# Kernel tuning notes

Hardware: AMD Instinct MI355X
Metric: run time of the kernel (lower is better)

Reference implementation:

```python
import jax, jax.numpy as jnp
import numpy as np

N_NODES = 50000
N_EDGES = 800000
D_IN = 256
D_HID = 256
N_LAYERS = 3
N_GRAPHS = 64
LN_EPS = 1e-5


def setup_inputs() -> dict:
    key = jax.random.key(0)
    ks = jax.random.split(key, 8)
    x = jax.random.normal(ks[0], (N_NODES, D_IN), dtype=jnp.float32)
    edge_index = jax.random.randint(ks[1], (2, N_EDGES), 0, N_NODES, dtype=jnp.int32)
    batch = jnp.sort(jax.random.randint(ks[2], (N_NODES,), 0, N_GRAPHS, dtype=jnp.int32))
    # GCNConv weights (glorot-ish) and biases; all layers are [D, D] since in_dim == hidden_dim
    scale = 1.0 / np.sqrt(D_IN)
    Ws = jax.random.normal(ks[3], (N_LAYERS, D_IN, D_HID), dtype=jnp.float32) * scale
    bs = jnp.zeros((N_LAYERS, D_HID), dtype=jnp.float32)
    gammas = jnp.ones((N_LAYERS, D_HID), dtype=jnp.float32)
    betas = jnp.zeros((N_LAYERS, D_HID), dtype=jnp.float32)
    return {"x": x, "edge_index": edge_index, "batch": batch,
            "Ws": Ws, "bs": bs, "gammas": gammas, "betas": betas}


def _gcn_conv(x, W, b, src, dst):
    # PyG GCNConv: h = xW; add self-loops; symmetric deg^{-1/2} normalization; scatter-add; + bias
    h = x @ W  # [N, D]
    deg = jnp.zeros((N_NODES,), dtype=x.dtype).at[dst].add(1.0) + 1.0  # +1 for self-loop
    dinv = jax.lax.rsqrt(deg)  # deg >= 1, safe
    coef = (dinv[src] * dinv[dst])[:, None]  # [E, 1]
    agg = jax.ops.segment_sum(h[src] * coef, dst, num_segments=N_NODES)
    agg = agg + h * (dinv * dinv)[:, None]  # self-loop contribution
    return agg + b


def _layer_norm(x, gamma, beta):
    mu = jnp.mean(x, axis=-1, keepdims=True)
    var = jnp.mean(jnp.square(x - mu), axis=-1, keepdims=True)
    return (x - mu) * jax.lax.rsqrt(var + LN_EPS) * gamma + beta


def reference(x, edge_index, batch, Ws, bs, gammas, betas):
    src, dst = edge_index[0], edge_index[1]
    h = x
    for l in range(N_LAYERS):
        h = _gcn_conv(h, Ws[l], bs[l], src, dst)
        h = _layer_norm(h, gammas[l], betas[l])
        h = jax.nn.relu(h)  # dropout is identity in eval mode
    # global mean pool over graphs
    sums = jax.ops.segment_sum(h, batch, num_segments=N_GRAPHS)  # [B, D]
    counts = jax.ops.segment_sum(jnp.ones((N_NODES,), dtype=h.dtype), batch, num_segments=N_GRAPHS)
    return sums / jnp.maximum(counts, 1.0)[:, None]
```

## Files before the change

### kernel.cpp

```cpp
#include <hip/hip_runtime.h>
#include <hip/hip_bf16.h>

#define N_NODES   50000
#define N_EDGES   800000
#define D         256
#define N_LAYERS  3
#define N_GRAPHS  64
#define LN_EPS    1e-5f
#define NB_SCAN   ((N_NODES + 255) / 256)

typedef __attribute__((ext_vector_type(8))) short bf16x8;
typedef __attribute__((ext_vector_type(4))) float f32x4;

__device__ __forceinline__ unsigned short f2bf(float f) {
    unsigned int u = __float_as_uint(f);
    unsigned int r = (u + 0x7FFFu + ((u >> 16) & 1u)) >> 16;
    return (unsigned short)r;
}
__device__ __forceinline__ float bf2f(unsigned short h) {
    return __uint_as_float(((unsigned int)h) << 16);
}

__global__ void k_xtobf_s(const float* __restrict__ x, const float* __restrict__ dinv,
                          unsigned short* __restrict__ xb) {
    int gid = blockIdx.x * blockDim.x + threadIdx.x;
    int base = gid * 8;
    if (base >= N_NODES * D) return;
    float sc = dinv[base >> 8];
    const float4* x4 = (const float4*)(x + base);
    float4 a = x4[0], b = x4[1];
    ushort4 lo, hi;
    lo.x = f2bf(a.x * sc); lo.y = f2bf(a.y * sc); lo.z = f2bf(a.z * sc); lo.w = f2bf(a.w * sc);
    hi.x = f2bf(b.x * sc); hi.y = f2bf(b.y * sc); hi.z = f2bf(b.z * sc); hi.w = f2bf(b.w * sc);
    ((ushort4*)(xb + base))[0] = lo;
    ((ushort4*)(xb + base))[1] = hi;
}

__global__ void k_wtrans(const float* __restrict__ W, unsigned short* __restrict__ Wbt) {
    int gid = blockIdx.x * blockDim.x + threadIdx.x;
    if (gid >= N_LAYERS * D * D) return;
    int l = gid >> 16;
    int rem = gid & 65535;
    int n = rem >> 8;
    int k = rem & 255;
    Wbt[(size_t)l * D * D + n * D + k] = f2bf(W[(size_t)l * D * D + k * D + n]);
}

__global__ void k_indeg(const int* __restrict__ dst, int* __restrict__ indeg) {
    int e = blockIdx.x * blockDim.x + threadIdx.x;
    if (e < N_EDGES) atomicAdd(&indeg[dst[e]], 1);
}

__global__ __launch_bounds__(256) void k_dinv_bsum(const int* __restrict__ indeg,
                                                   float* __restrict__ dinv,
                                                   int* __restrict__ bsum) {
    int b = blockIdx.x, t = threadIdx.x;
    int i = b * 256 + t;
    int v = (i < N_NODES) ? indeg[i] : 0;
    if (i < N_NODES) dinv[i] = rsqrtf((float)(v + 1));
    int s = v;
#pragma unroll
    for (int m = 32; m >= 1; m >>= 1) s += __shfl_xor(s, m);
    __shared__ int sh[4];
    if ((t & 63) == 0) sh[t >> 6] = s;
    __syncthreads();
    if (t == 0) bsum[b] = sh[0] + sh[1] + sh[2] + sh[3];
}

__global__ __launch_bounds__(256) void k_bscan_counts(const int* __restrict__ bsum,
                                                      int* __restrict__ bbase,
                                                      const int* __restrict__ batch,
                                                      int* __restrict__ counts) {
    int t = threadIdx.x;
    if (t < N_GRAPHS) {
        int g = t;
        int lo = 0, hi = N_NODES;
        while (lo < hi) { int mid = (lo + hi) >> 1; if (batch[mid] < g) lo = mid + 1; else hi = mid; }
        int start = lo;
        lo = 0; hi = N_NODES;
        int g1 = g + 1;
        while (lo < hi) { int mid = (lo + hi) >> 1; if (batch[mid] < g1) lo = mid + 1; else hi = mid; }
        counts[g] = lo - start;
    }
    __shared__ int s[256];
    int v = (t < NB_SCAN) ? bsum[t] : 0;
    s[t] = v;
    __syncthreads();
    for (int off = 1; off < 256; off <<= 1) {
        int tv = (t >= off) ? s[t - off] : 0;
        __syncthreads();
        s[t] += tv;
        __syncthreads();
    }
    if (t < NB_SCAN) bbase[t] = s[t] - v;
}

__global__ __launch_bounds__(256) void k_offsets(const int* __restrict__ indeg, const int* __restrict__ bbase,
                                                 int* __restrict__ offsets, int* __restrict__ cursor) {
    __shared__ int s[256];
    int b = blockIdx.x, t = threadIdx.x;
    int i = b * 256 + t;
    int v = (i < N_NODES) ? indeg[i] : 0;
    s[t] = v;
    __syncthreads();
    for (int off = 1; off < 256; off <<= 1) {
        int tv = (t >= off) ? s[t - off] : 0;
        __syncthreads();
        s[t] += tv;
        __syncthreads();
    }
    if (i < N_NODES) {
        int o = bbase[b] + s[t] - v;
        offsets[i] = o;
        cursor[i]  = o;
    }
}

__global__ void k_csr_fill(const int* __restrict__ src, const int* __restrict__ dst,
                           int* __restrict__ cursor, unsigned short* __restrict__ esrc) {
    int e = blockIdx.x * blockDim.x + threadIdx.x;
    if (e >= N_EDGES) return;
    int s = src[e], d = dst[e];
    int pos = atomicAdd(&cursor[d], 1);
    esrc[pos] = (unsigned short)s;
}

__global__ __launch_bounds__(256) void k_agg(const unsigned short* __restrict__ h,
                                             const int* __restrict__ offsets,
                                             const int* __restrict__ indeg,
                                             const float* __restrict__ dinv,
                                             const unsigned short* __restrict__ esrc,
                                             unsigned short* __restrict__ outA) {
    const int node = blockIdx.x * 4 + (threadIdx.x >> 6);
    const int lane = threadIdx.x & 63;
    if (node >= N_NODES) return;
    const int hw = lane >> 5;
    const int dl = lane & 31;
    const unsigned short* hp = h + dl * 8;

    float acc[8];
    if (hw == 0) {
        bf16x8 v = *(const bf16x8*)(hp + (size_t)node * 256);
#pragma unroll
        for (int j = 0; j < 8; ++j) acc[j] = bf2f((unsigned short)v[j]);
    } else {
#pragma unroll
        for (int j = 0; j < 8; ++j) acc[j] = 0.f;
    }

    const int beg = offsets[node];
    const int end = beg + indeg[node];
    int i = beg + hw;
    for (; i + 6 < end; i += 8) {
        int s0 = esrc[i];
        int s1 = esrc[i + 2];
        int s2 = esrc[i + 4];
        int s3 = esrc[i + 6];
        bf16x8 v0 = *(const bf16x8*)(hp + (size_t)s0 * 256);
        bf16x8 v1 = *(const bf16x8*)(hp + (size_t)s1 * 256);
        bf16x8 v2 = *(const bf16x8*)(hp + (size_t)s2 * 256);
        bf16x8 v3 = *(const bf16x8*)(hp + (size_t)s3 * 256);
#pragma unroll
        for (int j = 0; j < 8; ++j) acc[j] += bf2f((unsigned short)v0[j]);
#pragma unroll
        for (int j = 0; j < 8; ++j) acc[j] += bf2f((unsigned short)v1[j]);
#pragma unroll
        for (int j = 0; j < 8; ++j) acc[j] += bf2f((unsigned short)v2[j]);
#pragma unroll
        for (int j = 0; j < 8; ++j) acc[j] += bf2f((unsigned short)v3[j]);
    }
    for (; i < end; i += 2) {
        int s0 = esrc[i];
        bf16x8 v0 = *(const bf16x8*)(hp + (size_t)s0 * 256);
#pragma unroll
        for (int j = 0; j < 8; ++j) acc[j] += bf2f((unsigned short)v0[j]);
    }

#pragma unroll
    for (int j = 0; j < 8; ++j) acc[j] += __shfl_xor(acc[j], 32);

    if (hw == 0) {
        float sc = dinv[node];
        bf16x8 o;
#pragma unroll
        for (int j = 0; j < 8; ++j) o[j] = (short)f2bf(acc[j] * sc);
        *(bf16x8*)(outA + (size_t)node * 256 + dl * 8) = o;
    }
}

__global__ __launch_bounds__(512, 4) void k_gemm_ln(const unsigned short* __restrict__ A,
                                                    const unsigned short* __restrict__ Wbt,
                                                    const float* __restrict__ bias,
                                                    const float* __restrict__ gamma,
                                                    const float* __restrict__ beta,
                                                    const float* __restrict__ rowscale,
                                                    unsigned short* __restrict__ out) {
    __shared__ short alds[64 * 256];
    __shared__ float red[2][8][64];
    const int t = threadIdx.x;
    const int lane = t & 63;
    const int w = t >> 6;
    const int lrow = lane & 15;
    const int q = lane >> 4;
    const int ncb = w * 32;
    const int brow = blockIdx.x * 64;

#pragma unroll
    for (int it = 0; it < 4; ++it) {
        int L = it * 512 + t;
        int r = L >> 5;
        int c = L & 31;
        int row = brow + r; if (row >= N_NODES) row = N_NODES - 1;
        bf16x8 v = *(const bf16x8*)(A + (size_t)row * 256 + c * 8);
        *(bf16x8*)(alds + r * 256 + (c ^ (r & 7)) * 8) = v;
    }
    __syncthreads();

    f32x4 acc[4][2];
#pragma unroll
    for (int mt = 0; mt < 4; ++mt)
#pragma unroll
        for (int nt = 0; nt < 2; ++nt) acc[mt][nt] = (f32x4){0.f, 0.f, 0.f, 0.f};

    const unsigned short* wp0 = Wbt + (size_t)(ncb + lrow) * 256 + q * 8;
    const unsigned short* wp1 = Wbt + (size_t)(ncb + 16 + lrow) * 256 + q * 8;

#pragma unroll
    for (int kh = 0; kh < 2; ++kh) {
        bf16x8 wf0[4], wf1[4];
#pragma unroll
        for (int ks = 0; ks < 4; ++ks) {
            wf0[ks] = *(const bf16x8*)(wp0 + (kh * 4 + ks) * 32);
            wf1[ks] = *(const bf16x8*)(wp1 + (kh * 4 + ks) * 32);
        }
#pragma unroll
        for (int ks = 0; ks < 4; ++ks) {
            int kk = kh * 4 + ks;
            int cs = (kk * 4 + q) ^ (lrow & 7);
#pragma unroll
            for (int mt = 0; mt < 4; ++mt) {
                bf16x8 av = *(const bf16x8*)(alds + (mt * 16 + lrow) * 256 + cs * 8);
                acc[mt][0] = __builtin_amdgcn_mfma_f32_16x16x32_bf16(wf0[ks], av, acc[mt][0], 0, 0, 0);
                acc[mt][1] = __builtin_amdgcn_mfma_f32_16x16x32_bf16(wf1[ks], av, acc[mt][1], 0, 0, 0);
            }
        }
    }

    const float4* bias4 = (const float4*)bias;
#pragma unroll
    for (int mt = 0; mt < 4; ++mt) {
        float s = 0.f, s2 = 0.f;
#pragma unroll
        for (int nt = 0; nt < 2; ++nt) {
            float4 bv = bias4[w * 8 + nt * 4 + q];
#pragma unroll
            for (int r = 0; r < 4; ++r) {
                float v = acc[mt][nt][r] + ((const float*)&bv)[r];
                acc[mt][nt][r] = v;
                s += v;
                s2 += v * v;
            }
        }
        s  += __shfl_xor(s, 16);  s  += __shfl_xor(s, 32);
        s2 += __shfl_xor(s2, 16); s2 += __shfl_xor(s2, 32);
        if (lane < 16) {
            red[0][w][mt * 16 + lane] = s;
            red[1][w][mt * 16 + lane] = s2;
        }
    }
    __syncthreads();

    const float4* g4 = (const float4*)gamma;
    const float4* be4 = (const float4*)beta;
#pragma unroll
    for (int mt = 0; mt < 4; ++mt) {
        int r = mt * 16 + lrow;
        float s = 0.f, s2 = 0.f;
#pragma unroll
        for (int j = 0; j < 8; ++j) { s += red[0][j][r]; s2 += red[1][j][r]; }
        float mu = s * (1.0f / 256.0f);
        float var = s2 * (1.0f / 256.0f) - mu * mu;
        float rs = rsqrtf(var + LN_EPS);

        int row = brow + r;
        if (row < N_NODES) {
            float sc = (rowscale != nullptr) ? rowscale[row] : 1.0f;
#pragma unroll
            for (int nt = 0; nt < 2; ++nt) {
                float4 gv = g4[w * 8 + nt * 4 + q];
                float4 bev = be4[w * 8 + nt * 4 + q];
                ushort4 o;
                float v0 = fmaxf((acc[mt][nt][0] - mu) * rs * gv.x + bev.x, 0.f) * sc;
                float v1 = fmaxf((acc[mt][nt][1] - mu) * rs * gv.y + bev.y, 0.f) * sc;
                float v2 = fmaxf((acc[mt][nt][2] - mu) * rs * gv.z + bev.z, 0.f) * sc;
                float v3 = fmaxf((acc[mt][nt][3] - mu) * rs * gv.w + bev.w, 0.f) * sc;
                o.x = f2bf(v0); o.y = f2bf(v1); o.z = f2bf(v2); o.w = f2bf(v3);
                *(ushort4*)(out + (size_t)row * 256 + ncb + nt * 16 + q * 4) = o;
            }
        }
    }
}

__global__ __launch_bounds__(256) void k_pool(const unsigned short* __restrict__ h,
                                              const int* __restrict__ batch,
                                              float* __restrict__ sums) {
    __shared__ int sb[128];
    int t = threadIdx.x;
    int n0 = blockIdx.x * 128;
    int cnt = N_NODES - n0; if (cnt > 128) cnt = 128;
    if (cnt <= 0) return;
    if (t < cnt) sb[t] = batch[n0 + t];
    __syncthreads();

    float acc = 0.f;
    int g = sb[0];
    for (int i = 0; i < cnt; ++i) {
        int bg = sb[i];
        if (bg != g) {
            atomicAdd(&sums[g * 256 + t], acc);
            acc = 0.f;
            g = bg;
        }
        acc += bf2f(h[(size_t)(n0 + i) * 256 + t]);
    }
    atomicAdd(&sums[g * 256 + t], acc);
}

__global__ void k_finalize(const float* __restrict__ sums, const int* __restrict__ counts,
                           float* __restrict__ out) {
    int idx = blockIdx.x * blockDim.x + threadIdx.x;
    if (idx < N_GRAPHS * 256) {
        float c = (float)counts[idx >> 8];
        out[idx] = sums[idx] / fmaxf(c, 1.f);
    }
}

extern "C" void kernel_launch(void* const* d_in, const int* in_sizes, int n_in,
                              void* d_out, int out_size, void* d_ws, size_t ws_size,
                              hipStream_t stream) {
    const float* x     = (const float*)d_in[0];
    const int*   ei    = (const int*)d_in[1];
    const int*   batch = (const int*)d_in[2];
    const float* Ws    = (const float*)d_in[3];
    const float* bs    = (const float*)d_in[4];
    const float* gammas= (const float*)d_in[5];
    const float* betas = (const float*)d_in[6];
    float* out = (float*)d_out;

    const int* src = ei;
    const int* dst = ei + N_EDGES;

    char* p = (char*)d_ws;
    unsigned short* hbf   = (unsigned short*)p; p += (size_t)N_NODES * D * 2;
    unsigned short* aggx  = (unsigned short*)p; p += (size_t)N_NODES * D * 2;
    unsigned short* Wbt   = (unsigned short*)p; p += (size_t)N_LAYERS * D * D * 2;
    int*   indeg  = (int*)p;   p += (size_t)N_NODES * 4;
    int*   offs   = (int*)p;   p += (size_t)N_NODES * 4;
    int*   cursor = (int*)p;   p += (size_t)N_NODES * 4;
    float* dinv   = (float*)p; p += (size_t)N_NODES * 4;
    int*   bsum   = (int*)p;   p += (size_t)NB_SCAN * 4;
    int*   bbase  = (int*)p;   p += (size_t)NB_SCAN * 4;
    unsigned short* esrc = (unsigned short*)p; p += (size_t)N_EDGES * 2;
    float* sums   = (float*)p; p += (size_t)N_GRAPHS * D * 4;
    int*   counts = (int*)p;   p += (size_t)N_GRAPHS * 4;

    hipMemsetAsync(indeg, 0, (size_t)N_NODES * 4, stream);
    hipMemsetAsync(sums, 0, (size_t)N_GRAPHS * D * 4, stream);

    k_indeg <<<(N_EDGES + 255) / 256, 256, 0, stream>>>(dst, indeg);
    k_dinv_bsum<<<NB_SCAN, 256, 0, stream>>>(indeg, dinv, bsum);
    k_xtobf_s<<<(N_NODES * D / 8 + 255) / 256, 256, 0, stream>>>(x, dinv, hbf);
    k_wtrans<<<(N_LAYERS * D * D + 255) / 256, 256, 0, stream>>>(Ws, Wbt);
    k_bscan_counts<<<1, 256, 0, stream>>>(bsum, bbase, batch, counts);
    k_offsets<<<NB_SCAN, 256, 0, stream>>>(indeg, bbase, offs, cursor);
    k_csr_fill<<<(N_EDGES + 255) / 256, 256, 0, stream>>>(src, dst, cursor, esrc);

    const int agg_grid  = (N_NODES + 3) / 4;
    const int gemm_grid = (N_NODES + 63) / 64;
    for (int l = 0; l < N_LAYERS; ++l) {
        k_agg<<<agg_grid, 256, 0, stream>>>(hbf, offs, indeg, dinv, esrc, aggx);
        const float* rsc = (l == N_LAYERS - 1) ? nullptr : dinv;
        k_gemm_ln<<<gemm_grid, 512, 0, stream>>>(aggx, Wbt + (size_t)l * D * D,
                                                 bs + (size_t)l * D,
                                                 gammas + (size_t)l * D,
                                                 betas + (size_t)l * D, rsc, hbf);
    }

    k_pool<<<(N_NODES + 127) / 128, 256, 0, stream>>>(hbf, batch, sums);
    k_finalize<<<(N_GRAPHS * 256 + 255) / 256, 256, 0, stream>>>(sums, counts, out);
}
```

Baseline: 418.2 us.

## Store inter-layer activations as 8-bit floats to halve aggregation gather traffic

```diff
diff --git a/kernel.cpp b/kernel.cpp
--- a/kernel.cpp
+++ b/kernel.cpp
@@ -1,5 +1,6 @@
 #include <hip/hip_runtime.h>
 #include <hip/hip_bf16.h>
+#include <hip/hip_fp16.h>
 
 #define N_NODES   50000
 #define N_EDGES   800000
@@ -8,6 +9,7 @@
 #define N_GRAPHS  64
 #define LN_EPS    1e-5f
 #define NB_SCAN   ((N_NODES + 255) / 256)
+#define XT_THREADS (N_NODES * D / 8)
 
 typedef __attribute__((ext_vector_type(8))) short bf16x8;
 typedef __attribute__((ext_vector_type(4))) float f32x4;
@@ -21,29 +23,41 @@
     return __uint_as_float(((unsigned int)h) << 16);
 }
 
-__global__ void k_xtobf_s(const float* __restrict__ x, const float* __restrict__ dinv,
-                          unsigned short* __restrict__ xb) {
+__device__ __forceinline__ float f8tof_s(unsigned int b) {
+    unsigned short h = (unsigned short)(((b & 0x80u) << 8) | ((b & 0x7fu) << 7));
+    return __half2float(__ushort_as_half(h));
+}
+__device__ __forceinline__ unsigned int ftof8(float v) {
+    v = fminf(v, 448.f);
+    unsigned short hb = __half_as_ushort(__float2half(v * 0.00390625f));
+    hb = (unsigned short)(hb + 0x3F + ((hb >> 7) & 1));
+    return (unsigned int)((hb >> 7) & 0x7fu);
+}
+
+__global__ void k_convert(const float* __restrict__ x, const float* __restrict__ dinv,
+                          unsigned short* __restrict__ xb,
+                          const float* __restrict__ W, unsigned short* __restrict__ Wbt) {
     int gid = blockIdx.x * blockDim.x + threadIdx.x;
-    int base = gid * 8;
-    if (base >= N_NODES * D) return;
-    float sc = dinv[base >> 8];
-    const float4* x4 = (const float4*)(x + base);
-    float4 a = x4[0], b = x4[1];
-    ushort4 lo, hi;
-    lo.x = f2bf(a.x * sc); lo.y = f2bf(a.y * sc); lo.z = f2bf(a.z * sc); lo.w = f2bf(a.w * sc);
-    hi.x = f2bf(b.x * sc); hi.y = f2bf(b.y * sc); hi.z = f2bf(b.z * sc); hi.w = f2bf(b.w * sc);
-    ((ushort4*)(xb + base))[0] = lo;
-    ((ushort4*)(xb + base))[1] = hi;
-}
-
-__global__ void k_wtrans(const float* __restrict__ W, unsigned short* __restrict__ Wbt) {
-    int gid = blockIdx.x * blockDim.x + threadIdx.x;
-    if (gid >= N_LAYERS * D * D) return;
-    int l = gid >> 16;
-    int rem = gid & 65535;
-    int n = rem >> 8;
-    int k = rem & 255;
-    Wbt[(size_t)l * D * D + n * D + k] = f2bf(W[(size_t)l * D * D + k * D + n]);
+    if (gid < XT_THREADS) {
+        int base = gid * 8;
+        float sc = dinv[base >> 8];
+        const float4* x4 = (const float4*)(x + base);
+        float4 a = x4[0], b = x4[1];
+        ushort4 lo, hi;
+        lo.x = f2bf(a.x * sc); lo.y = f2bf(a.y * sc); lo.z = f2bf(a.z * sc); lo.w = f2bf(a.w * sc);
+        hi.x = f2bf(b.x * sc); hi.y = f2bf(b.y * sc); hi.z = f2bf(b.z * sc); hi.w = f2bf(b.w * sc);
+        ((ushort4*)(xb + base))[0] = lo;
+        ((ushort4*)(xb + base))[1] = hi;
+    } else {
+        int g2 = gid - XT_THREADS;
+        if (g2 < N_LAYERS * D * D) {
+            int l = g2 >> 16;
+            int rem = g2 & 65535;
+            int n = rem >> 8;
+            int k = rem & 255;
+            Wbt[(size_t)l * D * D + n * D + k] = f2bf(W[(size_t)l * D * D + k * D + n]);
+        }
+    }
 }
 
 __global__ void k_indeg(const int* __restrict__ dst, int* __restrict__ indeg) {
@@ -188,13 +202,78 @@
     }
 }
 
+__device__ __forceinline__ void f8acc(uint2 d, float* acc) {
+#pragma unroll
+    for (int j = 0; j < 4; ++j) acc[j]     += f8tof_s((d.x >> (8 * j)) & 0xffu);
+#pragma unroll
+    for (int j = 0; j < 4; ++j) acc[4 + j] += f8tof_s((d.y >> (8 * j)) & 0xffu);
+}
+
+__global__ __launch_bounds__(256) void k_agg_f8(const unsigned char* __restrict__ h8,
+                                                const int* __restrict__ offsets,
+                                                const int* __restrict__ indeg,
+                                                const float* __restrict__ dinv,
+                                                const unsigned short* __restrict__ esrc,
+                                                unsigned short* __restrict__ outA) {
+    const int node = blockIdx.x * 4 + (threadIdx.x >> 6);
+    const int lane = threadIdx.x & 63;
+    if (node >= N_NODES) return;
+    const int hw = lane >> 5;
+    const int dl = lane & 31;
+    const unsigned char* hp = h8 + dl * 8;
+
+    float acc[8];
+#pragma unroll
+    for (int j = 0; j < 8; ++j) acc[j] = 0.f;
+    if (hw == 0) {
+        uint2 d = *(const uint2*)(hp + (size_t)node * 256);
+        f8acc(d, acc);
+    }
+
+    const int beg = offsets[node];
+    const int end = beg + indeg[node];
+    int i = beg + hw;
+    for (; i + 6 < end; i += 8) {
+        int s0 = esrc[i];
+        int s1 = esrc[i + 2];
+        int s2 = esrc[i + 4];
+        int s3 = esrc[i + 6];
+        uint2 d0 = *(const uint2*)(hp + (size_t)s0 * 256);
+        uint2 d1 = *(const uint2*)(hp + (size_t)s1 * 256);
+        uint2 d2 = *(const uint2*)(hp + (size_t)s2 * 256);
+        uint2 d3 = *(const uint2*)(hp + (size_t)s3 * 256);
+        f8acc(d0, acc);
+        f8acc(d1, acc);
+        f8acc(d2, acc);
+        f8acc(d3, acc);
+    }
+    for (; i < end; i += 2) {
+        int s0 = esrc[i];
+        uint2 d0 = *(const uint2*)(hp + (size_t)s0 * 256);
+        f8acc(d0, acc);
+    }
+
+#pragma unroll
+    for (int j = 0; j < 8; ++j) acc[j] += __shfl_xor(acc[j], 32);
+
+    if (hw == 0) {
+        float sc = dinv[node] * 256.0f;
+        bf16x8 o;
+#pragma unroll
+        for (int j = 0; j < 8; ++j) o[j] = (short)f2bf(acc[j] * sc);
+        *(bf16x8*)(outA + (size_t)node * 256 + dl * 8) = o;
+    }
+}
+
+template<int MODE>
 __global__ __launch_bounds__(512, 4) void k_gemm_ln(const unsigned short* __restrict__ A,
                                                     const unsigned short* __restrict__ Wbt,
                                                     const float* __restrict__ bias,
                                                     const float* __restrict__ gamma,
                                                     const float* __restrict__ beta,
                                                     const float* __restrict__ rowscale,
-                                                    unsigned short* __restrict__ out) {
+                                                    unsigned short* __restrict__ outb,
+                                                    unsigned char* __restrict__ out8) {
     __shared__ short alds[64 * 256];
     __shared__ float red[2][8][64];
     const int t = threadIdx.x;
@@ -284,18 +363,24 @@
 
         int row = brow + r;
         if (row < N_NODES) {
-            float sc = (rowscale != nullptr) ? rowscale[row] : 1.0f;
 #pragma unroll
             for (int nt = 0; nt < 2; ++nt) {
                 float4 gv = g4[w * 8 + nt * 4 + q];
                 float4 bev = be4[w * 8 + nt * 4 + q];
-                ushort4 o;
-                float v0 = fmaxf((acc[mt][nt][0] - mu) * rs * gv.x + bev.x, 0.f) * sc;
-                float v1 = fmaxf((acc[mt][nt][1] - mu) * rs * gv.y + bev.y, 0.f) * sc;
-                float v2 = fmaxf((acc[mt][nt][2] - mu) * rs * gv.z + bev.z, 0.f) * sc;
-                float v3 = fmaxf((acc[mt][nt][3] - mu) * rs * gv.w + bev.w, 0.f) * sc;
-                o.x = f2bf(v0); o.y = f2bf(v1); o.z = f2bf(v2); o.w = f2bf(v3);
-                *(ushort4*)(out + (size_t)row * 256 + ncb + nt * 16 + q * 4) = o;
+                float v0 = fmaxf((acc[mt][nt][0] - mu) * rs * gv.x + bev.x, 0.f);
+                float v1 = fmaxf((acc[mt][nt][1] - mu) * rs * gv.y + bev.y, 0.f);
+                float v2 = fmaxf((acc[mt][nt][2] - mu) * rs * gv.z + bev.z, 0.f);
+                float v3 = fmaxf((acc[mt][nt][3] - mu) * rs * gv.w + bev.w, 0.f);
+                if (MODE == 0) {
+                    float sc = rowscale[row];
+                    unsigned int u = ftof8(v0 * sc) | (ftof8(v1 * sc) << 8)
+                                   | (ftof8(v2 * sc) << 16) | (ftof8(v3 * sc) << 24);
+                    *(unsigned int*)(out8 + (size_t)row * 256 + ncb + nt * 16 + q * 4) = u;
+                } else {
+                    ushort4 o;
+                    o.x = f2bf(v0); o.y = f2bf(v1); o.z = f2bf(v2); o.w = f2bf(v3);
+                    *(ushort4*)(outb + (size_t)row * 256 + ncb + nt * 16 + q * 4) = o;
+                }
             }
         }
     }
@@ -353,6 +438,7 @@
     char* p = (char*)d_ws;
     unsigned short* hbf   = (unsigned short*)p; p += (size_t)N_NODES * D * 2;
     unsigned short* aggx  = (unsigned short*)p; p += (size_t)N_NODES * D * 2;
+    unsigned char*  h8    = (unsigned char*)p;  p += (size_t)N_NODES * D;
     unsigned short* Wbt   = (unsigned short*)p; p += (size_t)N_LAYERS * D * D * 2;
     int*   indeg  = (int*)p;   p += (size_t)N_NODES * 4;
     int*   offs   = (int*)p;   p += (size_t)N_NODES * 4;
@@ -369,22 +455,26 @@
 
     k_indeg <<<(N_EDGES + 255) / 256, 256, 0, stream>>>(dst, indeg);
     k_dinv_bsum<<<NB_SCAN, 256, 0, stream>>>(indeg, dinv, bsum);
-    k_xtobf_s<<<(N_NODES * D / 8 + 255) / 256, 256, 0, stream>>>(x, dinv, hbf);
-    k_wtrans<<<(N_LAYERS * D * D + 255) / 256, 256, 0, stream>>>(Ws, Wbt);
+    k_convert<<<(XT_THREADS + N_LAYERS * D * D + 255) / 256, 256, 0, stream>>>(x, dinv, hbf, Ws, Wbt);
     k_bscan_counts<<<1, 256, 0, stream>>>(bsum, bbase, batch, counts);
     k_offsets<<<NB_SCAN, 256, 0, stream>>>(indeg, bbase, offs, cursor);
     k_csr_fill<<<(N_EDGES + 255) / 256, 256, 0, stream>>>(src, dst, cursor, esrc);
 
     const int agg_grid  = (N_NODES + 3) / 4;
     const int gemm_grid = (N_NODES + 63) / 64;
-    for (int l = 0; l < N_LAYERS; ++l) {
-        k_agg<<<agg_grid, 256, 0, stream>>>(hbf, offs, indeg, dinv, esrc, aggx);
-        const float* rsc = (l == N_LAYERS - 1) ? nullptr : dinv;
-        k_gemm_ln<<<gemm_grid, 512, 0, stream>>>(aggx, Wbt + (size_t)l * D * D,
-                                                 bs + (size_t)l * D,
-                                                 gammas + (size_t)l * D,
-                                                 betas + (size_t)l * D, rsc, hbf);
-    }
+
+    k_agg<<<agg_grid, 256, 0, stream>>>(hbf, offs, indeg, dinv, esrc, aggx);
+    k_gemm_ln<0><<<gemm_grid, 512, 0, stream>>>(aggx, Wbt, bs, gammas, betas, dinv, nullptr, h8);
+
+    k_agg_f8<<<agg_grid, 256, 0, stream>>>(h8, offs, indeg, dinv, esrc, aggx);
+    k_gemm_ln<0><<<gemm_grid, 512, 0, stream>>>(aggx, Wbt + (size_t)1 * D * D,
+                                                bs + 1 * D, gammas + 1 * D, betas + 1 * D,
+                                                dinv, nullptr, h8);
+
+    k_agg_f8<<<agg_grid, 256, 0, stream>>>(h8, offs, indeg, dinv, esrc, aggx);
+    k_gemm_ln<1><<<gemm_grid, 512, 0, stream>>>(aggx, Wbt + (size_t)2 * D * D,
+                                                bs + 2 * D, gammas + 2 * D, betas + 2 * D,
+                                                nullptr, hbf, nullptr);
 
     k_pool<<<(N_NODES + 127) / 128, 256, 0, stream>>>(hbf, batch, sums);
     k_finalize<<<(N_GRAPHS * 256 + 255) / 256, 256, 0, stream>>>(sums, counts, out);
```

Measured after the change: 424.6 us. Within noise of the previous version (+1.5%).
